# Performance work log

Measured on AMD Instinct MI355X. Metric: run time of the kernel, lower is better.

## Reference

```python
import jax, jax.numpy as jnp
import numpy as np

D_MODEL = 1024
NUM_HEADS = 16
ROPE_BASE = 10000.0


def _rope_sincos(T, head_dim, dtype):
    # angles[t, i] = t / base**(2i/head_dim), i in [0, head_dim//2)
    pos = jnp.arange(T, dtype=jnp.float32)[:, None]              # [T, 1]
    inv_freq = 1.0 / (ROPE_BASE ** (jnp.arange(0, head_dim, 2, dtype=jnp.float32) / head_dim))
    angles = pos * inv_freq                                       # [T, half]
    sin = jnp.sin(angles).astype(dtype)[None, :, None, :]         # [1, T, 1, half]
    cos = jnp.cos(angles).astype(dtype)[None, :, None, :]
    return sin, cos


def _apply_rope(x, sin, cos):
    # x: [B, T, H, head_dim]; deinterleave even/odd lanes, rotate, concat halves
    x1, x2 = x[..., ::2], x[..., 1::2]                            # [B, T, H, half] each
    return jnp.concatenate([x1 * cos - x2 * sin, x1 * sin + x2 * cos], axis=-1)


def setup_inputs() -> dict:
    key = jax.random.key(0)
    ks = jax.random.split(key, 5)
    B, T, D = 2, 2048, D_MODEL
    s = 0.02
    return {
        "x": jax.random.normal(ks[0], (B, T, D), dtype=jnp.float32),
        "w_qkv": jax.random.normal(ks[1], (3 * D, D), dtype=jnp.float32) * s,
        "b_qkv": jnp.zeros((3 * D,), dtype=jnp.float32),
        "w_out": jax.random.normal(ks[2], (D, D), dtype=jnp.float32) * s,
        "b_out": jnp.zeros((D,), dtype=jnp.float32),
    }


def reference(x, w_qkv, b_qkv, w_out, b_out):
    B, T, D = x.shape
    H = NUM_HEADS
    hd = D // H
    scale = hd ** -0.5

    qkv = (x @ w_qkv.T + b_qkv).reshape(B, T, 3, H, hd)
    q, k, v = qkv[:, :, 0], qkv[:, :, 1], qkv[:, :, 2]            # [B, T, H, hd]

    sin, cos = _rope_sincos(T, hd, x.dtype)
    q = _apply_rope(q, sin, cos)
    k = _apply_rope(k, sin, cos)

    scores = jnp.einsum("bthd,bshd->bhts", q, k) * scale          # [B, H, T, T]
    weights = jax.nn.softmax(scores, axis=-1)
    out = jnp.einsum("bhts,bshd->bthd", weights, v)               # [B, T, H, hd]
    out = out.reshape(B, T, D)
    return out @ w_out.T + b_out
```

## Files before the change

kernel.cpp:

```cpp
#include <hip/hip_runtime.h>
#include <cstdint>
#include <cstddef>

typedef __attribute__((ext_vector_type(8))) short short8;
typedef __attribute__((ext_vector_type(8))) __bf16 bf16x8;
typedef __attribute__((ext_vector_type(4))) float f32x4;
typedef __attribute__((ext_vector_type(16))) float f32x16;
typedef __attribute__((ext_vector_type(4))) unsigned int uint32x4;

#define LOG2E 1.44269504088896340736f

__device__ __forceinline__ unsigned short f2bf(float f) {
    unsigned int u = __builtin_bit_cast(unsigned int, f);
    u += 0x7fffu + ((u >> 16) & 1u);
    return (unsigned short)(u >> 16);
}

__device__ __forceinline__ f32x4 zero4() {
    f32x4 z; z.x = 0.f; z.y = 0.f; z.z = 0.f; z.w = 0.f; return z;
}
__device__ __forceinline__ f32x16 zero16() {
    f32x16 z;
    #pragma unroll
    for (int i = 0; i < 16; ++i) z[i] = 0.f;
    return z;
}

__device__ __forceinline__ f32x4 mfma16(short8 a, short8 b, f32x4 c) {
    return __builtin_amdgcn_mfma_f32_16x16x32_bf16(
        __builtin_bit_cast(bf16x8, a), __builtin_bit_cast(bf16x8, b), c, 0, 0, 0);
}
__device__ __forceinline__ f32x16 mfma32(short8 a, short8 b, f32x16 c) {
    return __builtin_amdgcn_mfma_f32_32x32x16_bf16(
        __builtin_bit_cast(bf16x8, a), __builtin_bit_cast(bf16x8, b), c, 0, 0, 0);
}

__device__ __forceinline__ unsigned int cvt_pk_bf16(float lo, float hi) {
    unsigned int r;
    asm("v_cvt_pk_bf16_f32 %0, %1, %2" : "=v"(r) : "v"(lo), "v"(hi));
    return r;
}

__device__ __forceinline__ uint2 permswap(unsigned x, unsigned y) {
#if __has_builtin(__builtin_amdgcn_permlane32_swap)
    auto r = __builtin_amdgcn_permlane32_swap(x, y, false, false);
    return make_uint2(r[0], r[1]);
#else
    int lane = threadIdx.x & 63;
    unsigned sy = __shfl_xor(y, 32), sx = __shfl_xor(x, 32);
    return make_uint2((lane < 32) ? x : sy, (lane < 32) ? sx : y);
#endif
}
__device__ __forceinline__ float red_max32(float v) {
    unsigned u = __builtin_bit_cast(unsigned, v);
    uint2 p = permswap(u, u);
    return fmaxf(__builtin_bit_cast(float, p.x), __builtin_bit_cast(float, p.y));
}

__device__ __forceinline__ void gload_lds16(const void* g, void* l, int lane) {
#if __has_builtin(__builtin_amdgcn_global_load_lds)
    __builtin_amdgcn_global_load_lds(
        (const __attribute__((address_space(1))) void*)g,
        (__attribute__((address_space(3))) void*)l, 16, 0, 0);
    (void)lane;
#else
    reinterpret_cast<int4*>(l)[lane] = *reinterpret_cast<const int4*>(g);
#endif
}

__global__ __launch_bounds__(256) void prep_kernel(
    const float* __restrict__ x, const float* __restrict__ wq,
    const float* __restrict__ wo,
    unsigned short* __restrict__ xb, unsigned short* __restrict__ wqb,
    unsigned short* __restrict__ wob, float2* __restrict__ tab) {
    const int S0 = 1048576, S1 = 786432, S2 = 262144;
    int i = blockIdx.x * 256 + threadIdx.x;
    const float* src; unsigned short* dst; int j;
    if (i < S0) { src = x; dst = xb; j = i; }
    else if (i < S0 + S1) { src = wq; dst = wqb; j = i - S0; }
    else if (i < S0 + S1 + S2) { src = wo; dst = wob; j = i - S0 - S1; }
    else {
        int idx = i - (S0 + S1 + S2);
        if (idx < 2048 * 32) {
            int t = idx >> 5, ii = idx & 31;
            float inv_freq = powf(10000.0f, -(float)ii / 32.0f);
            float ang = (float)t * inv_freq;
            tab[idx] = make_float2(cosf(ang), sinf(ang));
        }
        return;
    }
    float4 v = reinterpret_cast<const float4*>(src)[j];
    ushort4 o;
    o.x = f2bf(v.x); o.y = f2bf(v.y); o.z = f2bf(v.z); o.w = f2bf(v.w);
    reinterpret_cast<ushort4*>(dst)[j] = o;
}

__device__ __forceinline__ void gemm_mainloop_128x128(
    const unsigned short* __restrict__ A, const unsigned short* __restrict__ B,
    int K, int m0, int n0, unsigned short* As, unsigned short* Bs, f32x4 acc[2][4]) {
    int tid = threadIdx.x;
    int wave = tid >> 6, lane = tid & 63;
    int wm = wave >> 1, wn = wave & 1;
    int g = lane >> 4, c = lane & 15;
    const int NS = K >> 6;

    auto stage = [&](int buf, int k0) {
        #pragma unroll
        for (int i = 0; i < 2; ++i) {
            int call = wave * 2 + i;
            int s = call * 64 + lane;
            int row = s >> 3, c8 = s & 7;
            int csw = (c8 ^ (row & 7)) << 3;
            gload_lds16(A + (size_t)(m0 + row) * K + k0 + csw,
                        (char*)As + buf * 16384 + call * 1024, lane);
            gload_lds16(B + (size_t)(n0 + row) * K + k0 + csw,
                        (char*)Bs + buf * 16384 + call * 1024, lane);
        }
    };

    stage(0, 0);

    #pragma unroll 1
    for (int t = 0; t < NS; ++t) {
        int cur = t & 1;
        asm volatile("s_waitcnt vmcnt(0) lgkmcnt(0)" ::: "memory");
        __builtin_amdgcn_s_barrier();
        __builtin_amdgcn_sched_barrier(0);
        if (t + 1 < NS) stage(cur ^ 1, (t + 1) * 64);

        const char* Ac = (const char*)As + cur * 16384;
        const char* Bc = (const char*)Bs + cur * 16384;
        #pragma unroll
        for (int kg = 0; kg < 2; ++kg) {
            short8 af[2], bfr[4];
            #pragma unroll
            for (int mt = 0; mt < 2; ++mt) {
                int row = wm * 32 + mt * 16 + c;
                af[mt] = *reinterpret_cast<const short8*>(Ac +
                    ((row * 128 + kg * 64 + g * 16) ^ ((row & 7) << 4)));
            }
            #pragma unroll
            for (int nt = 0; nt < 4; ++nt) {
                int row = wn * 64 + nt * 16 + c;
                bfr[nt] = *reinterpret_cast<const short8*>(Bc +
                    ((row * 128 + kg * 64 + g * 16) ^ ((row & 7) << 4)));
            }
            __builtin_amdgcn_s_setprio(1);
            #pragma unroll
            for (int mt = 0; mt < 2; ++mt)
                #pragma unroll
                for (int nt = 0; nt < 4; ++nt)
                    acc[mt][nt] = mfma16(af[mt], bfr[nt], acc[mt][nt]);
            __builtin_amdgcn_s_setprio(0);
        }
    }
}

__global__ __launch_bounds__(512, 2) void qkv_gemm_kernel(
    const unsigned short* __restrict__ X, const unsigned short* __restrict__ W,
    const float* __restrict__ bias, const float2* __restrict__ tab,
    unsigned short* __restrict__ q, unsigned short* __restrict__ k,
    unsigned short* __restrict__ vt) {
    __shared__ unsigned short As[2][128 * 64];
    __shared__ unsigned short Bs[2][128 * 64];
    const int K = 1024;
    const float SCL = 0.125f * LOG2E;
    int flat = blockIdx.x + 24 * blockIdx.y;
    int swzb = (flat & 7) * 96 + (flat >> 3);
    int m0 = (swzb / 24) * 128, n0 = (swzb % 24) * 128;
    f32x4 acc[2][4];
    #pragma unroll
    for (int i = 0; i < 2; ++i)
        #pragma unroll
        for (int j = 0; j < 4; ++j) acc[i][j] = zero4();

    gemm_mainloop_128x128(X, W, K, m0, n0, &As[0][0], &Bs[0][0], acc);

    int tid = threadIdx.x;
    int wave = tid >> 6, lane = tid & 63;
    int wm = wave >> 1, wn = wave & 1;
    int g = lane >> 4, c = lane & 15;
    int mbase = m0 + wm * 32, nbase = n0 + wn * 64;
    #pragma unroll
    for (int mt = 0; mt < 2; ++mt) {
        #pragma unroll
        for (int nt = 0; nt < 4; ++nt) {
            f32x4 a = acc[mt][nt];
            int n = nbase + nt * 16 + c;
            int s = n >> 10;
            int h = (n >> 6) & 15;
            int d = n & 63;
            float bn = bias[n];
            #pragma unroll
            for (int r = 0; r < 4; ++r) {
                int m = mbase + mt * 16 + g * 4 + r;
                int bb = m >> 11, t = m & 2047;
                float val = a[r] + bn;
                float partner = __shfl_xor(val, 1);
                int bh = bb * 16 + h;
                if (s == 2) {
                    vt[((size_t)bh * 64 + d) * 2048 + t] = f2bf(val);
                } else {
                    int i2 = d >> 1;
                    float2 cs = tab[t * 32 + i2];
                    float outv; int dout;
                    if ((d & 1) == 0) { outv = val * cs.x - partner * cs.y; dout = i2; }
                    else              { outv = partner * cs.y + val * cs.x; dout = 32 + i2; }
                    if (s == 0) outv *= SCL;
                    (s == 0 ? q : k)[((size_t)bh * 2048 + t) * 64 + dout] = f2bf(outv);
                }
            }
        }
    }
}

__global__ __launch_bounds__(512, 2) void attn_kernel(
    const unsigned short* __restrict__ Q, const unsigned short* __restrict__ Kin,
    const unsigned short* __restrict__ VT, unsigned short* __restrict__ O) {
    __shared__ int4 smem4[65536 / 16];
    char* smem = (char*)smem4;
    const int T = 2048, NT = 16;
    int flat = blockIdx.x + 16 * blockIdx.y;
    int swzb = (flat & 7) * 64 + (flat >> 3);
    int bh = swzb >> 4;
    int qt = swzb & 15;
    int tid = threadIdx.x, wave = tid >> 6, lane = tid & 63;
    int lam = lane & 31, hi = lane >> 5;
    int pair = wave & 3, half = wave >> 2;
    int q = qt * 128 + pair * 32 + lam;

    const unsigned short* Qb = Q + ((size_t)bh * T + q) * 64;
    const unsigned short* Kb = Kin + (size_t)bh * T * 64;
    const unsigned short* VTb = VT + (size_t)bh * 64 * T;

    uint32x4 qtmp[4];
    #pragma unroll
    for (int c4 = 0; c4 < 4; ++c4)
        qtmp[c4] = *reinterpret_cast<const uint32x4*>(Qb + c4 * 16 + hi * 8);
    #pragma unroll
    for (int c4 = 0; c4 < 4; ++c4)
        asm volatile("" : "+v"(qtmp[c4]));
    short8 qf[4];
    #pragma unroll
    for (int c4 = 0; c4 < 4; ++c4) qf[c4] = __builtin_bit_cast(short8, qtmp[c4]);

    short8 ones;
    #pragma unroll
    for (int i = 0; i < 8; ++i) ones[i] = (short)0x3F80;

    f32x16 o0 = zero16(), o1 = zero16(), lacc = zero16();
    float m_run = -1e30f;
    int swz = (lam & 7) << 4;

    char* Ks0 = smem + half * 16384;
    char* Vs0 = smem + 32768 + half * 16384;

    auto stage = [&](int buf, int t) {
        int j0 = half * 1024 + t * 64;
        #pragma unroll
        for (int i = 0; i < 2; ++i) {
            int call = pair * 2 + i;
            int s = call * 64 + lane;
            int row = s >> 3, c8 = s & 7;
            int csw = (c8 ^ (row & 7)) << 3;
            gload_lds16(Kb + (size_t)(j0 + row) * 64 + csw,
                        Ks0 + buf * 8192 + call * 1024, lane);
            gload_lds16(VTb + (size_t)row * T + j0 + csw,
                        Vs0 + buf * 8192 + call * 1024, lane);
        }
    };

    stage(0, 0);

    #pragma unroll 1
    for (int t = 0; t < NT; ++t) {
        int cur = t & 1;
        asm volatile("s_waitcnt vmcnt(0) lgkmcnt(0)" ::: "memory");
        __builtin_amdgcn_s_barrier();
        __builtin_amdgcn_sched_barrier(0);
        if (t + 1 < NT) stage(cur ^ 1, t + 1);

        const char* Kc = Ks0 + cur * 8192;
        const char* Vc = Vs0 + cur * 8192;

        f32x16 s0 = zero16(), s1 = zero16();
        __builtin_amdgcn_s_setprio(1);
        #pragma unroll
        for (int c4 = 0; c4 < 4; ++c4) {
            int col = c4 * 32 + hi * 16;
            short8 kf0 = *reinterpret_cast<const short8*>(Kc + ((lam * 128 + col) ^ swz));
            s0 = mfma32(kf0, qf[c4], s0);
            short8 kf1 = *reinterpret_cast<const short8*>(Kc + (((lam + 32) * 128 + col) ^ swz));
            s1 = mfma32(kf1, qf[c4], s1);
        }
        __builtin_amdgcn_s_setprio(0);

        float tm = fmaxf(s0[0], s1[0]);
        #pragma unroll
        for (int r = 1; r < 16; ++r) tm = fmaxf(tm, fmaxf(s0[r], s1[r]));
        float tmax = red_max32(tm);
        if (__any(tmax - m_run > 8.0f)) {
            float mnew = fmaxf(m_run, tmax);
            float alpha = exp2f(m_run - mnew);
            m_run = mnew;
            #pragma unroll
            for (int r = 0; r < 16; ++r) {
                o0[r] *= alpha; o1[r] *= alpha; lacc[r] *= alpha;
            }
        }
        float p0[16], p1[16];
        #pragma unroll
        for (int r = 0; r < 16; ++r) p0[r] = exp2f(s0[r] - m_run);
        #pragma unroll
        for (int r = 0; r < 16; ++r) p1[r] = exp2f(s1[r] - m_run);

        short8 pa[4];
        #pragma unroll
        for (int blk = 0; blk < 2; ++blk) {
            const float* p = blk ? p1 : p0;
            #pragma unroll
            for (int jt = 0; jt < 2; ++jt) {
                unsigned a0 = cvt_pk_bf16(p[jt * 8 + 0], p[jt * 8 + 1]);
                unsigned a1 = cvt_pk_bf16(p[jt * 8 + 2], p[jt * 8 + 3]);
                unsigned b0 = cvt_pk_bf16(p[jt * 8 + 4], p[jt * 8 + 5]);
                unsigned b1 = cvt_pk_bf16(p[jt * 8 + 6], p[jt * 8 + 7]);
                uint2 pr0 = permswap(a0, b0);
                uint2 pr1 = permswap(a1, b1);
                uint4 w;
                w.x = pr0.x;
                w.y = pr1.x;
                w.z = pr0.y;
                w.w = pr1.y;
                pa[blk * 2 + jt] = __builtin_bit_cast(short8, w);
            }
        }

        __builtin_amdgcn_s_setprio(1);
        #pragma unroll
        for (int jt = 0; jt < 4; ++jt) {
            int col = jt * 32 + hi * 16;
            short8 vf0 = *reinterpret_cast<const short8*>(Vc + ((lam * 128 + col) ^ swz));
            o0 = mfma32(vf0, pa[jt], o0);
            short8 vf1 = *reinterpret_cast<const short8*>(Vc + (((lam + 32) * 128 + col) ^ swz));
            o1 = mfma32(vf1, pa[jt], o1);
            lacc = mfma32(ones, pa[jt], lacc);
        }
        __builtin_amdgcn_s_setprio(0);
    }

    float l_run = lacc[0];

    __syncthreads();
    float* pb = (float*)(smem + pair * 8704);
    if (half) {
        #pragma unroll
        for (int r = 0; r < 16; ++r) {
            pb[lane * 34 + r] = o0[r];
            pb[lane * 34 + 16 + r] = o1[r];
        }
        pb[lane * 34 + 32] = m_run;
        pb[lane * 34 + 33] = l_run;
    }
    __syncthreads();
    if (half) return;

    float mb = pb[lane * 34 + 32], lb = pb[lane * 34 + 33];
    float m = fmaxf(m_run, mb);
    float wa = exp2f(m_run - m), wb = exp2f(mb - m);
    float l = l_run * wa + lb * wb;
    float rinv = 1.0f / l;
    #pragma unroll
    for (int r = 0; r < 16; ++r) {
        o0[r] = o0[r] * wa + pb[lane * 34 + r] * wb;
        o1[r] = o1[r] * wa + pb[lane * 34 + 16 + r] * wb;
    }

    int b_ = bh >> 4, h_ = bh & 15;
    unsigned short* Orow = O + ((size_t)(b_ * 2048) + q) * 1024 + h_ * 64;
    #pragma unroll
    for (int rq = 0; rq < 4; ++rq) {
        ushort4 w0, w1;
        w0.x = f2bf(o0[rq * 4 + 0] * rinv);
        w0.y = f2bf(o0[rq * 4 + 1] * rinv);
        w0.z = f2bf(o0[rq * 4 + 2] * rinv);
        w0.w = f2bf(o0[rq * 4 + 3] * rinv);
        w1.x = f2bf(o1[rq * 4 + 0] * rinv);
        w1.y = f2bf(o1[rq * 4 + 1] * rinv);
        w1.z = f2bf(o1[rq * 4 + 2] * rinv);
        w1.w = f2bf(o1[rq * 4 + 3] * rinv);
        int d0 = rq * 8 + hi * 4;
        *reinterpret_cast<ushort4*>(Orow + d0) = w0;
        *reinterpret_cast<ushort4*>(Orow + 32 + d0) = w1;
    }
}

__global__ __launch_bounds__(512, 2) void out_gemm_kernel(
    const unsigned short* __restrict__ Aattn, const unsigned short* __restrict__ W,
    const float* __restrict__ bias, float* __restrict__ out) {
    __shared__ unsigned short As[2][128 * 64];
    __shared__ unsigned short Bs[2][128 * 64];
    const int K = 1024, N = 1024;
    int flat = blockIdx.x + 8 * blockIdx.y;
    int swzb = (flat & 7) * 32 + (flat >> 3);
    int m0 = (swzb >> 3) * 128, n0 = (swzb & 7) * 128;
    f32x4 acc[2][4];
    #pragma unroll
    for (int i = 0; i < 2; ++i)
        #pragma unroll
        for (int j = 0; j < 4; ++j) acc[i][j] = zero4();

    gemm_mainloop_128x128(Aattn, W, K, m0, n0, &As[0][0], &Bs[0][0], acc);

    int tid = threadIdx.x;
    int wave = tid >> 6, lane = tid & 63;
    int wm = wave >> 1, wn = wave & 1;
    int g = lane >> 4, c = lane & 15;
    int mbase = m0 + wm * 32, nbase = n0 + wn * 64;
    #pragma unroll
    for (int mt = 0; mt < 2; ++mt)
        #pragma unroll
        for (int nt = 0; nt < 4; ++nt) {
            int n = nbase + nt * 16 + c;
            float bn = bias[n];
            #pragma unroll
            for (int r = 0; r < 4; ++r) {
                int m = mbase + mt * 16 + g * 4 + r;
                out[(size_t)m * N + n] = acc[mt][nt][r] + bn;
            }
        }
}

extern "C" void kernel_launch(void* const* d_in, const int* in_sizes, int n_in,
                              void* d_out, int out_size, void* d_ws, size_t ws_size,
                              hipStream_t stream) {
    (void)in_sizes; (void)n_in; (void)out_size; (void)ws_size;
    const float* x     = (const float*)d_in[0];
    const float* w_qkv = (const float*)d_in[1];
    const float* b_qkv = (const float*)d_in[2];
    const float* w_out = (const float*)d_in[3];
    const float* b_out = (const float*)d_in[4];
    float* out = (float*)d_out;

    const int B = 2, T = 2048, D = 1024;
    const int M = B * T;
    const size_t MB = 1024 * 1024;

    char* ws = (char*)d_ws;
    unsigned short* xb    = (unsigned short*)(ws);
    unsigned short* wqkvb = (unsigned short*)(ws + 8 * MB);
    unsigned short* woutb = (unsigned short*)(ws + 14 * MB);
    unsigned short* qb    = (unsigned short*)(ws + 16 * MB);
    unsigned short* kb    = (unsigned short*)(ws + 24 * MB);
    unsigned short* vtb   = (unsigned short*)(ws + 32 * MB);
    unsigned short* attnb = (unsigned short*)(ws + 40 * MB);
    float2* tab           = (float2*)(ws + 48 * MB);

    prep_kernel<<<dim3((2097152 + 65536) / 256), dim3(256), 0, stream>>>(
        x, w_qkv, w_out, xb, wqkvb, woutb, tab);
    qkv_gemm_kernel<<<dim3(3 * D / 128, M / 128), dim3(512), 0, stream>>>(xb, wqkvb, b_qkv, tab, qb, kb, vtb);
    attn_kernel<<<dim3(T / 128, B * 16), dim3(512), 0, stream>>>(qb, kb, vtb, attnb);
    out_gemm_kernel<<<dim3(D / 128, M / 128), dim3(512), 0, stream>>>(attnb, woutb, b_out, out);
}
```

Before: 153.2 us.

## Retile QKV and output GEMMs to 128x192 and 64x128 for fuller waves

Turns the GEMM main loop into a template over block and wave-grid shape. The QKV projection now uses 128x192 tiles, giving 512 blocks, and the output projection uses 64x128 tiles, also giving 512 blocks, with 1D grids and an XCD-aware block swizzle. The intent is to balance occupancy across the 256 CUs and reduce tail effects. The change also drops the lgkmcnt wait before the barrier in the GEMM and attention loops, which relies on the LDS reads having already completed at that point.

```diff
diff --git a/kernel.cpp b/kernel.cpp
--- a/kernel.cpp
+++ b/kernel.cpp
@@ -95,26 +95,38 @@
     reinterpret_cast<ushort4*>(dst)[j] = o;
 }
 
-__device__ __forceinline__ void gemm_mainloop_128x128(
+template<int BM, int BN, int WMG, int WNG>
+__device__ __forceinline__ void gemm_mainloop(
     const unsigned short* __restrict__ A, const unsigned short* __restrict__ B,
-    int K, int m0, int n0, unsigned short* As, unsigned short* Bs, f32x4 acc[2][4]) {
+    int K, int m0, int n0, char* As, char* Bs,
+    f32x4 (&acc)[BM / (WMG * 16)][BN / (WNG * 16)]) {
+    constexpr int MT = BM / (WMG * 16), NTT = BN / (WNG * 16);
+    constexpr int CA = BM / 64, CB = BN / 64;
+    constexpr int ABUF = BM * 128, BBUF = BN * 128;
     int tid = threadIdx.x;
     int wave = tid >> 6, lane = tid & 63;
-    int wm = wave >> 1, wn = wave & 1;
+    int wm = wave / WNG, wn = wave % WNG;
     int g = lane >> 4, c = lane & 15;
     const int NS = K >> 6;
 
     auto stage = [&](int buf, int k0) {
         #pragma unroll
-        for (int i = 0; i < 2; ++i) {
-            int call = wave * 2 + i;
+        for (int i = 0; i < CA; ++i) {
+            int call = wave * CA + i;
             int s = call * 64 + lane;
             int row = s >> 3, c8 = s & 7;
             int csw = (c8 ^ (row & 7)) << 3;
             gload_lds16(A + (size_t)(m0 + row) * K + k0 + csw,
-                        (char*)As + buf * 16384 + call * 1024, lane);
+                        As + buf * ABUF + call * 1024, lane);
+        }
+        #pragma unroll
+        for (int i = 0; i < CB; ++i) {
+            int call = wave * CB + i;
+            int s = call * 64 + lane;
+            int row = s >> 3, c8 = s & 7;
+            int csw = (c8 ^ (row & 7)) << 3;
             gload_lds16(B + (size_t)(n0 + row) * K + k0 + csw,
-                        (char*)Bs + buf * 16384 + call * 1024, lane);
+                        Bs + buf * BBUF + call * 1024, lane);
         }
     };
 
@@ -123,33 +135,33 @@
     #pragma unroll 1
     for (int t = 0; t < NS; ++t) {
         int cur = t & 1;
-        asm volatile("s_waitcnt vmcnt(0) lgkmcnt(0)" ::: "memory");
+        asm volatile("s_waitcnt vmcnt(0)" ::: "memory");
         __builtin_amdgcn_s_barrier();
         __builtin_amdgcn_sched_barrier(0);
         if (t + 1 < NS) stage(cur ^ 1, (t + 1) * 64);
 
-        const char* Ac = (const char*)As + cur * 16384;
-        const char* Bc = (const char*)Bs + cur * 16384;
+        const char* Ac = As + cur * ABUF;
+        const char* Bc = Bs + cur * BBUF;
         #pragma unroll
         for (int kg = 0; kg < 2; ++kg) {
-            short8 af[2], bfr[4];
-            #pragma unroll
-            for (int mt = 0; mt < 2; ++mt) {
-                int row = wm * 32 + mt * 16 + c;
+            short8 af[MT], bfr[NTT];
+            #pragma unroll
+            for (int mt = 0; mt < MT; ++mt) {
+                int row = wm * (BM / WMG) + mt * 16 + c;
                 af[mt] = *reinterpret_cast<const short8*>(Ac +
                     ((row * 128 + kg * 64 + g * 16) ^ ((row & 7) << 4)));
             }
             #pragma unroll
-            for (int nt = 0; nt < 4; ++nt) {
-                int row = wn * 64 + nt * 16 + c;
+            for (int nt = 0; nt < NTT; ++nt) {
+                int row = wn * (BN / WNG) + nt * 16 + c;
                 bfr[nt] = *reinterpret_cast<const short8*>(Bc +
                     ((row * 128 + kg * 64 + g * 16) ^ ((row & 7) << 4)));
             }
             __builtin_amdgcn_s_setprio(1);
             #pragma unroll
-            for (int mt = 0; mt < 2; ++mt)
+            for (int mt = 0; mt < MT; ++mt)
                 #pragma unroll
-                for (int nt = 0; nt < 4; ++nt)
+                for (int nt = 0; nt < NTT; ++nt)
                     acc[mt][nt] = mfma16(af[mt], bfr[nt], acc[mt][nt]);
             __builtin_amdgcn_s_setprio(0);
         }
@@ -161,30 +173,29 @@
     const float* __restrict__ bias, const float2* __restrict__ tab,
     unsigned short* __restrict__ q, unsigned short* __restrict__ k,
     unsigned short* __restrict__ vt) {
-    __shared__ unsigned short As[2][128 * 64];
-    __shared__ unsigned short Bs[2][128 * 64];
+    __shared__ char smem[80 * 1024];
     const int K = 1024;
     const float SCL = 0.125f * LOG2E;
-    int flat = blockIdx.x + 24 * blockIdx.y;
-    int swzb = (flat & 7) * 96 + (flat >> 3);
-    int m0 = (swzb / 24) * 128, n0 = (swzb % 24) * 128;
-    f32x4 acc[2][4];
+    int flat = blockIdx.x;
+    int swzb = (flat & 7) * 64 + (flat >> 3);
+    int m0 = (swzb >> 4) * 128, n0 = (swzb & 15) * 192;
+    f32x4 acc[2][6];
     #pragma unroll
     for (int i = 0; i < 2; ++i)
         #pragma unroll
-        for (int j = 0; j < 4; ++j) acc[i][j] = zero4();
-
-    gemm_mainloop_128x128(X, W, K, m0, n0, &As[0][0], &Bs[0][0], acc);
+        for (int j = 0; j < 6; ++j) acc[i][j] = zero4();
+
+    gemm_mainloop<128, 192, 4, 2>(X, W, K, m0, n0, smem, smem + 32768, acc);
 
     int tid = threadIdx.x;
     int wave = tid >> 6, lane = tid & 63;
     int wm = wave >> 1, wn = wave & 1;
     int g = lane >> 4, c = lane & 15;
-    int mbase = m0 + wm * 32, nbase = n0 + wn * 64;
+    int mbase = m0 + wm * 32, nbase = n0 + wn * 96;
     #pragma unroll
     for (int mt = 0; mt < 2; ++mt) {
         #pragma unroll
-        for (int nt = 0; nt < 4; ++nt) {
+        for (int nt = 0; nt < 6; ++nt) {
             f32x4 a = acc[mt][nt];
             int n = nbase + nt * 16 + c;
             int s = n >> 10;
@@ -275,7 +286,7 @@
     #pragma unroll 1
     for (int t = 0; t < NT; ++t) {
         int cur = t & 1;
-        asm volatile("s_waitcnt vmcnt(0) lgkmcnt(0)" ::: "memory");
+        asm volatile("s_waitcnt vmcnt(0)" ::: "memory");
         __builtin_amdgcn_s_barrier();
         __builtin_amdgcn_sched_barrier(0);
         if (t + 1 < NT) stage(cur ^ 1, t + 1);
@@ -397,29 +408,28 @@
 __global__ __launch_bounds__(512, 2) void out_gemm_kernel(
     const unsigned short* __restrict__ Aattn, const unsigned short* __restrict__ W,
     const float* __restrict__ bias, float* __restrict__ out) {
-    __shared__ unsigned short As[2][128 * 64];
-    __shared__ unsigned short Bs[2][128 * 64];
+    __shared__ char smem[48 * 1024];
     const int K = 1024, N = 1024;
-    int flat = blockIdx.x + 8 * blockIdx.y;
-    int swzb = (flat & 7) * 32 + (flat >> 3);
-    int m0 = (swzb >> 3) * 128, n0 = (swzb & 7) * 128;
-    f32x4 acc[2][4];
+    int flat = blockIdx.x;
+    int swzb = (flat & 7) * 64 + (flat >> 3);
+    int m0 = (swzb & 63) * 64, n0 = (swzb >> 6) * 128;
+    f32x4 acc[2][2];
     #pragma unroll
     for (int i = 0; i < 2; ++i)
         #pragma unroll
-        for (int j = 0; j < 4; ++j) acc[i][j] = zero4();
-
-    gemm_mainloop_128x128(Aattn, W, K, m0, n0, &As[0][0], &Bs[0][0], acc);
+        for (int j = 0; j < 2; ++j) acc[i][j] = zero4();
+
+    gemm_mainloop<64, 128, 2, 4>(Aattn, W, K, m0, n0, smem, smem + 16384, acc);
 
     int tid = threadIdx.x;
     int wave = tid >> 6, lane = tid & 63;
-    int wm = wave >> 1, wn = wave & 1;
+    int wm = wave >> 2, wn = wave & 3;
     int g = lane >> 4, c = lane & 15;
-    int mbase = m0 + wm * 32, nbase = n0 + wn * 64;
+    int mbase = m0 + wm * 32, nbase = n0 + wn * 32;
     #pragma unroll
     for (int mt = 0; mt < 2; ++mt)
         #pragma unroll
-        for (int nt = 0; nt < 4; ++nt) {
+        for (int nt = 0; nt < 2; ++nt) {
             int n = nbase + nt * 16 + c;
             float bn = bias[n];
             #pragma unroll
@@ -444,6 +454,7 @@
     const int B = 2, T = 2048, D = 1024;
     const int M = B * T;
     const size_t MB = 1024 * 1024;
+    (void)D; (void)M;
 
     char* ws = (char*)d_ws;
     unsigned short* xb    = (unsigned short*)(ws);
@@ -457,7 +468,7 @@
 
     prep_kernel<<<dim3((2097152 + 65536) / 256), dim3(256), 0, stream>>>(
         x, w_qkv, w_out, xb, wqkvb, woutb, tab);
-    qkv_gemm_kernel<<<dim3(3 * D / 128, M / 128), dim3(512), 0, stream>>>(xb, wqkvb, b_qkv, tab, qb, kb, vtb);
+    qkv_gemm_kernel<<<dim3(512), dim3(512), 0, stream>>>(xb, wqkvb, b_qkv, tab, qb, kb, vtb);
     attn_kernel<<<dim3(T / 128, B * 16), dim3(512), 0, stream>>>(qb, kb, vtb, attnb);
-    out_gemm_kernel<<<dim3(D / 128, M / 128), dim3(512), 0, stream>>>(attnb, woutb, b_out, out);
-}
+    out_gemm_kernel<<<dim3(512), dim3(512), 0, stream>>>(attnb, woutb, b_out, out);
+}
```

Result: faster. 143.9 us (-6.1%).
